# Optimization experiments

Measured on AMD Instinct MI355X. Metric: run time of the kernel, lower is better.

## Reference

```python
import jax, jax.numpy as jnp
import numpy as np

QUERY_DIM = 512
KEY_DIM = 512
NUM_HEADS = 16
HEAD_DIM = QUERY_DIM // NUM_HEADS


def setup_inputs() -> dict:
    key = jax.random.key(0)
    ks = jax.random.split(key, 10)
    B, T, S = 4, 2048, 2048
    s_q = 1.0 / np.sqrt(QUERY_DIM)
    s_k = 1.0 / np.sqrt(KEY_DIM)
    return {
        "x": jax.random.normal(ks[0], (B, T, QUERY_DIM), dtype=jnp.float32),
        "context": jax.random.normal(ks[1], (B, S, KEY_DIM), dtype=jnp.float32),
        "Wq": jax.random.normal(ks[2], (QUERY_DIM, QUERY_DIM), dtype=jnp.float32) * s_q,
        "bq": jnp.zeros((QUERY_DIM,), dtype=jnp.float32),
        "Wk": jax.random.normal(ks[3], (KEY_DIM, QUERY_DIM), dtype=jnp.float32) * s_k,
        "bk": jnp.zeros((QUERY_DIM,), dtype=jnp.float32),
        "Wv": jax.random.normal(ks[4], (KEY_DIM, QUERY_DIM), dtype=jnp.float32) * s_k,
        "bv": jnp.zeros((QUERY_DIM,), dtype=jnp.float32),
        "Wo": jax.random.normal(ks[5], (QUERY_DIM, QUERY_DIM), dtype=jnp.float32) * s_q,
        "bo": jnp.zeros((QUERY_DIM,), dtype=jnp.float32),
    }


def reference(x, context, Wq, bq, Wk, bk, Wv, bv, Wo, bo):
    B, T, C = x.shape
    S = context.shape[1]
    H, D = NUM_HEADS, HEAD_DIM
    scale = D ** -0.5
    # projections -> [B, H, T/S, D]
    q = (x @ Wq + bq).reshape(B, T, H, D).transpose(0, 2, 1, 3)
    k = (context @ Wk + bk).reshape(B, S, H, D).transpose(0, 2, 1, 3)
    v = (context @ Wv + bv).reshape(B, S, H, D).transpose(0, 2, 1, 3)
    # explicit attention matrix [B, H, T, S] (faithful to the unfused original)
    attn = jnp.einsum("bhtd,bhsd->bhts", q, k) * scale
    attn = jax.nn.softmax(attn, axis=-1)  # dropout is identity in eval mode
    out = jnp.einsum("bhts,bhsd->bhtd", attn, v)
    out = out.transpose(0, 2, 1, 3).reshape(B, T, C)
    return out @ Wo + bo
```

## Files before the change

### kernel.cpp

```cpp
#include <hip/hip_runtime.h>
#include <hip/hip_bf16.h>
#include <cmath>

typedef __bf16 bf16;
typedef __bf16 bf16x4 __attribute__((ext_vector_type(4)));
typedef __bf16 bf16x8 __attribute__((ext_vector_type(8)));
typedef float floatx4 __attribute__((ext_vector_type(4)));

#define MFMA_BF16(a, b, c) __builtin_amdgcn_mfma_f32_16x16x32_bf16((a), (b), (c), 0, 0, 0)

#if defined(__has_builtin)
#if __has_builtin(__builtin_amdgcn_global_load_lds)
#define HAVE_GLL 1
#endif
#endif

__device__ __forceinline__ void stage16(const bf16* g, bf16* ldsbase, int lane) {
#ifdef HAVE_GLL
    __builtin_amdgcn_global_load_lds((const __attribute__((address_space(1))) unsigned int*)g,
                                     (__attribute__((address_space(3))) unsigned int*)ldsbase,
                                     16, 0, 0);
#else
    *(int4*)(ldsbase + lane * 8) = *(const int4*)g;
#endif
}

__device__ __forceinline__ int detect_bf16(const void* x) {
    const unsigned short* u = (const unsigned short*)x;
    const int lane = threadIdx.x & 63;
    const unsigned short w0 = u[4 * lane], w1 = u[4 * lane + 2];
    const int e0 = (w0 >> 7) & 0xFF, e1 = (w1 >> 7) & 0xFF;
    const unsigned long long b0 = __ballot(e0 >= 96 && e0 <= 158);
    const unsigned long long b1 = __ballot(e1 >= 96 && e1 <= 158);
    return (__popcll(b0) + __popcll(b1)) >= 90;
}

struct PrepArgs {
    const void* x;
    const void* ctx;
    const void* W[4];
    const void* bias[4];
    bf16* xc;
    bf16* ctxc;
    bf16* WT[4];
    bf16* biasc;
};

__global__ __launch_bounds__(256) void prep(PrepArgs a) {
    const int tid = threadIdx.x;
    const int f = detect_bf16(a.x);
    const int bid = blockIdx.x;
    if (bid < 1024) {
        const int w = bid >> 8, tileid = bid & 255;
        const int bx = tileid & 15, by = tileid >> 4;
        const void* __restrict__ in = a.W[w];
        bf16* __restrict__ out = a.WT[w];
        __shared__ bf16 tile[32][33];
        const int tx = tid & 31, ty = tid >> 5;
        const int x = bx * 32 + tx;
        const int y0 = by * 32;
#pragma unroll
        for (int yy = ty; yy < 32; yy += 8) {
            const size_t idx = (size_t)(y0 + yy) * 512 + x;
            const float v = f ? (float)((const bf16*)in)[idx] : ((const float*)in)[idx];
            tile[yy][tx] = (bf16)v;
        }
        __syncthreads();
        const int xo = by * 32 + tx;
        const int y1 = bx * 32;
#pragma unroll
        for (int yy = ty; yy < 32; yy += 8)
            out[(size_t)(y1 + yy) * 512 + xo] = tile[tx][yy];
    } else if (bid < 5120) {
        const int seg = (bid >= 3072);
        const void* src = seg ? a.ctx : a.x;
        bf16* dst = seg ? a.ctxc : a.xc;
        const int off = (bid - (seg ? 3072 : 1024)) * 256 + tid;
        if (f) {
            ((int4*)dst)[off] = ((const int4*)src)[off];
        } else {
            const float4 p = ((const float4*)src)[2 * off];
            const float4 q = ((const float4*)src)[2 * off + 1];
            bf16x8 o;
            o[0] = (bf16)p.x; o[1] = (bf16)p.y; o[2] = (bf16)p.z; o[3] = (bf16)p.w;
            o[4] = (bf16)q.x; o[5] = (bf16)q.y; o[6] = (bf16)q.z; o[7] = (bf16)q.w;
            *(bf16x8*)(dst + (size_t)off * 8) = o;
        }
    } else {
        for (int e = tid; e < 2048; e += 256) {
            const int seg = e >> 9, off = e & 511;
            const float v =
                f ? (float)((const bf16*)a.bias[seg])[off] : ((const float*)a.bias[seg])[off];
            a.biasc[seg * 512 + off] = (bf16)v;
        }
    }
}

struct QkvArgs {
    const bf16* A[3];
    const bf16* Wt[3];
    const bf16* bias;
    bf16* out[3];
    float scale[3];
};

__global__ __launch_bounds__(256) void gemm_qkv(QkvArgs a) {
    __shared__ __align__(16) bf16 lA[128 * 32];
    __shared__ __align__(16) bf16 lB[128 * 32];
    const int z = blockIdx.z;
    const bf16* __restrict__ A = a.A[z];
    const bf16* __restrict__ Wt = a.Wt[z];
    const int tid = threadIdx.x, wave = tid >> 6, lane = tid & 63;
    const int qd = lane >> 4, j = lane & 15;
    const int m0 = blockIdx.x * 128, n0 = blockIdx.y * 128;
    const int wrow = (wave & 1) * 64, wcol = (wave >> 1) * 64;
    const int srow = wave * 16 + (lane >> 2);
    const int scol = (lane & 3) * 8;
    const bf16* agp = A + (size_t)(m0 + srow) * 512 + scol;
    const bf16* bgp = Wt + (size_t)(n0 + srow) * 512 + scol;
    bf16* lA0 = lA + wave * 512;
    bf16* lB0 = lB + wave * 512;

    floatx4 acc[4][4] = {};

    for (int k0 = 0; k0 < 512; k0 += 32) {
        stage16(agp + k0, lA0, lane);
        stage16(agp + k0 + (size_t)64 * 512, lA0 + 64 * 32, lane);
        stage16(bgp + k0, lB0, lane);
        stage16(bgp + k0 + (size_t)64 * 512, lB0 + 64 * 32, lane);
        __syncthreads();
        bf16x8 af[4], bfr[4];
#pragma unroll
        for (int i = 0; i < 4; ++i) {
            af[i] = *(const bf16x8*)(lA + (wrow + i * 16 + j) * 32 + qd * 8);
            bfr[i] = *(const bf16x8*)(lB + (wcol + i * 16 + j) * 32 + qd * 8);
        }
        if (z < 2) {
#pragma unroll
            for (int nt = 0; nt < 4; ++nt)
#pragma unroll
                for (int rf = 0; rf < 4; ++rf)
                    acc[nt][rf] = MFMA_BF16(bfr[nt], af[rf], acc[nt][rf]);
        } else {
#pragma unroll
            for (int rf = 0; rf < 4; ++rf)
#pragma unroll
                for (int nt = 0; nt < 4; ++nt)
                    acc[rf][nt] = MFMA_BF16(af[rf], bfr[nt], acc[rf][nt]);
        }
        __syncthreads();
    }

    const float scale = a.scale[z];
    const bf16* bias = a.bias + z * 512;
    bf16* __restrict__ C = a.out[z];
    if (z < 2) {
#pragma unroll
        for (int nt = 0; nt < 4; ++nt) {
            const int nb = n0 + wcol + nt * 16 + qd * 4;
            const bf16x4 bv4 = *(const bf16x4*)(bias + nb);
            const int h = nb >> 5, d0 = nb & 31;
#pragma unroll
            for (int rf = 0; rf < 4; ++rf) {
                const int m = m0 + wrow + rf * 16 + j;
                const int bb = m >> 11, t = m & 2047;
                bf16x4 pk;
#pragma unroll
                for (int r = 0; r < 4; ++r)
                    pk[r] = (bf16)((acc[nt][rf][r] + (float)bv4[r]) * scale);
                *(bf16x4*)(&C[(((size_t)bb * 16 + h) * 2048 + t) * 32 + d0]) = pk;
            }
        }
    } else {
#pragma unroll
        for (int nt = 0; nt < 4; ++nt) {
            const int n = n0 + wcol + nt * 16 + j;
            const float bv = (float)bias[n];
            const int h = n >> 5, d = n & 31;
#pragma unroll
            for (int rf = 0; rf < 4; ++rf) {
                const int t0 = m0 + wrow + rf * 16 + qd * 4;
                const int bb = t0 >> 11, s = t0 & 2047;
                bf16x4 pk;
#pragma unroll
                for (int r = 0; r < 4; ++r) pk[r] = (bf16)(acc[rf][nt][r] + bv);
                *(bf16x4*)(&C[(((size_t)bb * 16 + h) * 32 + d) * 2048 + s]) = pk;
            }
        }
    }
}

__global__ __launch_bounds__(256) void gemm_out(const bf16* __restrict__ A,
                                                const bf16* __restrict__ Wt,
                                                const bf16* __restrict__ bias,
                                                void* __restrict__ C,
                                                const void* __restrict__ xorig) {
    __shared__ __align__(16) bf16 lA[128 * 32];
    __shared__ __align__(16) bf16 lB[128 * 32];
    const int oflag = detect_bf16(xorig);
    const int tid = threadIdx.x, wave = tid >> 6, lane = tid & 63;
    const int qd = lane >> 4, j = lane & 15;
    const int m0 = blockIdx.x * 128, n0 = blockIdx.y * 128;
    const int wrow = (wave & 1) * 64, wcol = (wave >> 1) * 64;
    const int srow = wave * 16 + (lane >> 2);
    const int scol = (lane & 3) * 8;
    const bf16* agp = A + (size_t)(m0 + srow) * 512 + scol;
    const bf16* bgp = Wt + (size_t)(n0 + srow) * 512 + scol;
    bf16* lA0 = lA + wave * 512;
    bf16* lB0 = lB + wave * 512;

    floatx4 acc[4][4] = {};

    for (int k0 = 0; k0 < 512; k0 += 32) {
        stage16(agp + k0, lA0, lane);
        stage16(agp + k0 + (size_t)64 * 512, lA0 + 64 * 32, lane);
        stage16(bgp + k0, lB0, lane);
        stage16(bgp + k0 + (size_t)64 * 512, lB0 + 64 * 32, lane);
        __syncthreads();
        bf16x8 af[4], bfr[4];
#pragma unroll
        for (int i = 0; i < 4; ++i) {
            af[i] = *(const bf16x8*)(lA + (wrow + i * 16 + j) * 32 + qd * 8);
            bfr[i] = *(const bf16x8*)(lB + (wcol + i * 16 + j) * 32 + qd * 8);
        }
#pragma unroll
        for (int nt = 0; nt < 4; ++nt)
#pragma unroll
            for (int rf = 0; rf < 4; ++rf)
                acc[nt][rf] = MFMA_BF16(bfr[nt], af[rf], acc[nt][rf]);
        __syncthreads();
    }

#pragma unroll
    for (int nt = 0; nt < 4; ++nt) {
        const int nb = n0 + wcol + nt * 16 + qd * 4;
        const bf16x4 bv4 = *(const bf16x4*)(bias + nb);
#pragma unroll
        for (int rf = 0; rf < 4; ++rf) {
            const int m = m0 + wrow + rf * 16 + j;
            if (oflag) {
                bf16x4 pk;
#pragma unroll
                for (int r = 0; r < 4; ++r) pk[r] = (bf16)(acc[nt][rf][r] + (float)bv4[r]);
                *(bf16x4*)((bf16*)C + (size_t)m * 512 + nb) = pk;
            } else {
                float4 v;
                v.x = acc[nt][rf][0] + (float)bv4[0];
                v.y = acc[nt][rf][1] + (float)bv4[1];
                v.z = acc[nt][rf][2] + (float)bv4[2];
                v.w = acc[nt][rf][3] + (float)bv4[3];
                *(float4*)((float*)C + (size_t)m * 512 + nb) = v;
            }
        }
    }
}

__global__ __launch_bounds__(256) void attn_kernel(const bf16* __restrict__ Q,
                                                   const bf16* __restrict__ Kh,
                                                   const bf16* __restrict__ Vt,
                                                   bf16* __restrict__ O) {
    const int tid = threadIdx.x;
    const int wave = tid >> 6, lane = tid & 63;
    const int qd = lane >> 4, j = lane & 15;
    const int bh = blockIdx.y;
    const int b = bh >> 4, h = bh & 15;
    const int tw = blockIdx.x * 256 + wave * 64;

    __shared__ __align__(16) bf16 lP[4][64 * 68];
    bf16* lp = lP[wave];

    const bf16* qbase = Q + ((size_t)bh * 2048 + tw) * 32;
    const bf16* kbase = Kh + (size_t)bh * 2048 * 32;
    const bf16* vbase = Vt + (size_t)bh * 32 * 2048;

    bf16x8 qf[4];
#pragma unroll
    for (int tf = 0; tf < 4; ++tf)
        qf[tf] = *(const bf16x8*)(qbase + (size_t)(tf * 16 + j) * 32 + qd * 8);

    const floatx4 zero = {0.f, 0.f, 0.f, 0.f};
    floatx4 oacc[4][2] = {};
    float lrow[4] = {0.f, 0.f, 0.f, 0.f};

    bf16x8 kc[4], vc[4], kn[4], vn[4], vp[4];

    auto loadK = [&](int s0, bf16x8* k) {
#pragma unroll
        for (int sf = 0; sf < 4; ++sf)
            k[sf] = *(const bf16x8*)(kbase + (size_t)(s0 + sf * 16 + j) * 32 + qd * 8);
    };
    auto loadV = [&](int s0, bf16x8* v) {
#pragma unroll
        for (int dt = 0; dt < 2; ++dt)
#pragma unroll
            for (int kk = 0; kk < 2; ++kk)
                v[dt * 2 + kk] =
                    *(const bf16x8*)(vbase + (size_t)(dt * 16 + j) * 2048 + s0 + kk * 32 + qd * 8);
    };
    auto qk_exp_write = [&](bf16x8* k) {
#pragma unroll
        for (int sf = 0; sf < 4; ++sf)
#pragma unroll
            for (int tf = 0; tf < 4; ++tf) {
                const floatx4 sc = MFMA_BF16(k[sf], qf[tf], zero);
                float e0 = __builtin_amdgcn_exp2f(sc[0]);
                float e1 = __builtin_amdgcn_exp2f(sc[1]);
                float e2 = __builtin_amdgcn_exp2f(sc[2]);
                float e3 = __builtin_amdgcn_exp2f(sc[3]);
                lrow[tf] += (e0 + e1) + (e2 + e3);
                bf16x4 pk;
                pk[0] = (bf16)e0; pk[1] = (bf16)e1; pk[2] = (bf16)e2; pk[3] = (bf16)e3;
                *(bf16x4*)(lp + (tf * 16 + j) * 68 + sf * 16 + qd * 4) = pk;
            }
    };
    auto pv = [&](bf16x8* v) {
#pragma unroll
        for (int rf = 0; rf < 4; ++rf)
#pragma unroll
            for (int kk = 0; kk < 2; ++kk) {
                const bf16x8 pf = *(const bf16x8*)(lp + (rf * 16 + j) * 68 + kk * 32 + qd * 8);
#pragma unroll
                for (int dt = 0; dt < 2; ++dt)
                    oacc[rf][dt] = MFMA_BF16(pf, v[dt * 2 + kk], oacc[rf][dt]);
            }
    };

    loadK(0, kc);
    loadV(0, vc);
    qk_exp_write(kc);
#pragma unroll
    for (int i = 0; i < 4; ++i) vp[i] = vc[i];
    loadK(64, kc);
    loadV(64, vc);

    for (int it = 1; it < 32; ++it) {
        const int sn = (it + 1) * 64 & 2047;
        loadK(sn, kn);
        loadV(sn, vn);
        pv(vp);
        qk_exp_write(kc);
#pragma unroll
        for (int i = 0; i < 4; ++i) { vp[i] = vc[i]; kc[i] = kn[i]; vc[i] = vn[i]; }
    }
    pv(vp);

    float lr[4];
#pragma unroll
    for (int tf = 0; tf < 4; ++tf) {
        float v = lrow[tf];
        v += __shfl_xor(v, 16);
        v += __shfl_xor(v, 32);
        lr[tf] = v;
    }

#pragma unroll
    for (int rf = 0; rf < 4; ++rf)
#pragma unroll
        for (int r = 0; r < 4; ++r) {
            const float den = __shfl(lr[rf], qd * 4 + r);
            const float inv = 1.0f / den;
            const int t = tw + rf * 16 + qd * 4 + r;
#pragma unroll
            for (int dt = 0; dt < 2; ++dt)
                O[((size_t)b * 2048 + t) * 512 + h * 32 + dt * 16 + j] =
                    (bf16)(oacc[rf][dt][r] * inv);
        }
}

extern "C" void kernel_launch(void* const* d_in, const int* in_sizes, int n_in, void* d_out,
                              int out_size, void* d_ws, size_t ws_size, hipStream_t stream) {
    char* ws = (char*)d_ws;
    bf16* wqT = (bf16*)(ws + 1048576);
    bf16* wkT = (bf16*)(ws + 1572864);
    bf16* wvT = (bf16*)(ws + 2097152);
    bf16* woT = (bf16*)(ws + 2621440);
    bf16* biasc = (bf16*)(ws + 3145728);
    bf16* xc = (bf16*)(ws + 4194304);
    bf16* ctxc = (bf16*)(ws + 12582912);
    bf16* qws = (bf16*)(ws + 20971520);
    bf16* kws = (bf16*)(ws + 29360128);
    bf16* vtws = (bf16*)(ws + 37748736);
    bf16* aws = xc;

    PrepArgs pa;
    pa.x = d_in[0]; pa.ctx = d_in[1];
    pa.W[0] = d_in[2]; pa.W[1] = d_in[4]; pa.W[2] = d_in[6]; pa.W[3] = d_in[8];
    pa.bias[0] = d_in[3]; pa.bias[1] = d_in[5]; pa.bias[2] = d_in[7]; pa.bias[3] = d_in[9];
    pa.xc = xc; pa.ctxc = ctxc;
    pa.WT[0] = wqT; pa.WT[1] = wkT; pa.WT[2] = wvT; pa.WT[3] = woT;
    pa.biasc = biasc;
    prep<<<5121, 256, 0, stream>>>(pa);

    QkvArgs qa;
    qa.A[0] = xc; qa.A[1] = ctxc; qa.A[2] = ctxc;
    qa.Wt[0] = wqT; qa.Wt[1] = wkT; qa.Wt[2] = wvT;
    qa.bias = biasc;
    qa.out[0] = qws; qa.out[1] = kws; qa.out[2] = vtws;
    qa.scale[0] = 0.2550348593f; qa.scale[1] = 1.0f; qa.scale[2] = 1.0f;
    gemm_qkv<<<dim3(64, 4, 3), 256, 0, stream>>>(qa);

    attn_kernel<<<dim3(8, 64), 256, 0, stream>>>(qws, kws, vtws, aws);

    gemm_out<<<dim3(64, 4), 256, 0, stream>>>(aws, woT, biasc + 3 * 512, d_out, d_in[0]);
}
```

Before: 218.0 us.

## Split attention over the key dimension and merge partials inside the output GEMM

```diff
diff --git a/kernel.cpp b/kernel.cpp
--- a/kernel.cpp
+++ b/kernel.cpp
@@ -72,20 +72,17 @@
         for (int yy = ty; yy < 32; yy += 8)
             out[(size_t)(y1 + yy) * 512 + xo] = tile[tx][yy];
     } else if (bid < 5120) {
+        if (f) return;
         const int seg = (bid >= 3072);
         const void* src = seg ? a.ctx : a.x;
         bf16* dst = seg ? a.ctxc : a.xc;
         const int off = (bid - (seg ? 3072 : 1024)) * 256 + tid;
-        if (f) {
-            ((int4*)dst)[off] = ((const int4*)src)[off];
-        } else {
-            const float4 p = ((const float4*)src)[2 * off];
-            const float4 q = ((const float4*)src)[2 * off + 1];
-            bf16x8 o;
-            o[0] = (bf16)p.x; o[1] = (bf16)p.y; o[2] = (bf16)p.z; o[3] = (bf16)p.w;
-            o[4] = (bf16)q.x; o[5] = (bf16)q.y; o[6] = (bf16)q.z; o[7] = (bf16)q.w;
-            *(bf16x8*)(dst + (size_t)off * 8) = o;
-        }
+        const float4 p = ((const float4*)src)[2 * off];
+        const float4 q = ((const float4*)src)[2 * off + 1];
+        bf16x8 o;
+        o[0] = (bf16)p.x; o[1] = (bf16)p.y; o[2] = (bf16)p.z; o[3] = (bf16)p.w;
+        o[4] = (bf16)q.x; o[5] = (bf16)q.y; o[6] = (bf16)q.z; o[7] = (bf16)q.w;
+        *(bf16x8*)(dst + (size_t)off * 8) = o;
     } else {
         for (int e = tid; e < 2048; e += 256) {
             const int seg = e >> 9, off = e & 511;
@@ -97,7 +94,9 @@
 }
 
 struct QkvArgs {
-    const bf16* A[3];
+    const void* xraw;
+    const void* ctxraw;
+    const bf16* Aconv[3];
     const bf16* Wt[3];
     const bf16* bias;
     bf16* out[3];
@@ -108,7 +107,9 @@
     __shared__ __align__(16) bf16 lA[128 * 32];
     __shared__ __align__(16) bf16 lB[128 * 32];
     const int z = blockIdx.z;
-    const bf16* __restrict__ A = a.A[z];
+    const int f = detect_bf16(a.xraw);
+    const bf16* __restrict__ A =
+        f ? (const bf16*)(z == 0 ? a.xraw : a.ctxraw) : a.Aconv[z];
     const bf16* __restrict__ Wt = a.Wt[z];
     const int tid = threadIdx.x, wave = tid >> 6, lane = tid & 63;
     const int qd = lane >> 4, j = lane & 15;
@@ -190,81 +191,20 @@
     }
 }
 
-__global__ __launch_bounds__(256) void gemm_out(const bf16* __restrict__ A,
-                                                const bf16* __restrict__ Wt,
-                                                const bf16* __restrict__ bias,
-                                                void* __restrict__ C,
-                                                const void* __restrict__ xorig) {
-    __shared__ __align__(16) bf16 lA[128 * 32];
-    __shared__ __align__(16) bf16 lB[128 * 32];
-    const int oflag = detect_bf16(xorig);
-    const int tid = threadIdx.x, wave = tid >> 6, lane = tid & 63;
-    const int qd = lane >> 4, j = lane & 15;
-    const int m0 = blockIdx.x * 128, n0 = blockIdx.y * 128;
-    const int wrow = (wave & 1) * 64, wcol = (wave >> 1) * 64;
-    const int srow = wave * 16 + (lane >> 2);
-    const int scol = (lane & 3) * 8;
-    const bf16* agp = A + (size_t)(m0 + srow) * 512 + scol;
-    const bf16* bgp = Wt + (size_t)(n0 + srow) * 512 + scol;
-    bf16* lA0 = lA + wave * 512;
-    bf16* lB0 = lB + wave * 512;
-
-    floatx4 acc[4][4] = {};
-
-    for (int k0 = 0; k0 < 512; k0 += 32) {
-        stage16(agp + k0, lA0, lane);
-        stage16(agp + k0 + (size_t)64 * 512, lA0 + 64 * 32, lane);
-        stage16(bgp + k0, lB0, lane);
-        stage16(bgp + k0 + (size_t)64 * 512, lB0 + 64 * 32, lane);
-        __syncthreads();
-        bf16x8 af[4], bfr[4];
-#pragma unroll
-        for (int i = 0; i < 4; ++i) {
-            af[i] = *(const bf16x8*)(lA + (wrow + i * 16 + j) * 32 + qd * 8);
-            bfr[i] = *(const bf16x8*)(lB + (wcol + i * 16 + j) * 32 + qd * 8);
-        }
-#pragma unroll
-        for (int nt = 0; nt < 4; ++nt)
-#pragma unroll
-            for (int rf = 0; rf < 4; ++rf)
-                acc[nt][rf] = MFMA_BF16(bfr[nt], af[rf], acc[nt][rf]);
-        __syncthreads();
-    }
-
-#pragma unroll
-    for (int nt = 0; nt < 4; ++nt) {
-        const int nb = n0 + wcol + nt * 16 + qd * 4;
-        const bf16x4 bv4 = *(const bf16x4*)(bias + nb);
-#pragma unroll
-        for (int rf = 0; rf < 4; ++rf) {
-            const int m = m0 + wrow + rf * 16 + j;
-            if (oflag) {
-                bf16x4 pk;
-#pragma unroll
-                for (int r = 0; r < 4; ++r) pk[r] = (bf16)(acc[nt][rf][r] + (float)bv4[r]);
-                *(bf16x4*)((bf16*)C + (size_t)m * 512 + nb) = pk;
-            } else {
-                float4 v;
-                v.x = acc[nt][rf][0] + (float)bv4[0];
-                v.y = acc[nt][rf][1] + (float)bv4[1];
-                v.z = acc[nt][rf][2] + (float)bv4[2];
-                v.w = acc[nt][rf][3] + (float)bv4[3];
-                *(float4*)((float*)C + (size_t)m * 512 + nb) = v;
-            }
-        }
-    }
-}
-
 __global__ __launch_bounds__(256) void attn_kernel(const bf16* __restrict__ Q,
                                                    const bf16* __restrict__ Kh,
                                                    const bf16* __restrict__ Vt,
-                                                   bf16* __restrict__ O) {
+                                                   bf16* __restrict__ Opart,
+                                                   float* __restrict__ lpart)
+{
     const int tid = threadIdx.x;
     const int wave = tid >> 6, lane = tid & 63;
     const int qd = lane >> 4, j = lane & 15;
-    const int bh = blockIdx.y;
+    const int bh = blockIdx.x;
     const int b = bh >> 4, h = bh & 15;
-    const int tw = blockIdx.x * 256 + wave * 64;
+    const int tw = blockIdx.y * 256 + wave * 64;
+    const int z = blockIdx.z;
+    const int sbase = z * 1024;
 
     __shared__ __align__(16) bf16 lP[4][64 * 68];
     bf16* lp = lP[wave];
@@ -325,16 +265,16 @@
             }
     };
 
-    loadK(0, kc);
-    loadV(0, vc);
+    loadK(sbase, kc);
+    loadV(sbase, vc);
     qk_exp_write(kc);
 #pragma unroll
     for (int i = 0; i < 4; ++i) vp[i] = vc[i];
-    loadK(64, kc);
-    loadV(64, vc);
-
-    for (int it = 1; it < 32; ++it) {
-        const int sn = (it + 1) * 64 & 2047;
+    loadK(sbase + 64, kc);
+    loadV(sbase + 64, vc);
+
+    for (int it = 1; it < 16; ++it) {
+        const int sn = sbase + (((it + 1) * 64) & 1023);
         loadK(sn, kn);
         loadV(sn, vn);
         pv(vp);
@@ -353,23 +293,108 @@
         lr[tf] = v;
     }
 
+    bf16* op = Opart + (size_t)z * 8192 * 512;
+    float* lo = lpart + (size_t)z * 131072 + (size_t)bh * 2048 + tw;
+    if (qd == 0) {
+#pragma unroll
+        for (int tf = 0; tf < 4; ++tf) lo[tf * 16 + j] = lr[tf];
+    }
 #pragma unroll
     for (int rf = 0; rf < 4; ++rf)
 #pragma unroll
         for (int r = 0; r < 4; ++r) {
-            const float den = __shfl(lr[rf], qd * 4 + r);
-            const float inv = 1.0f / den;
             const int t = tw + rf * 16 + qd * 4 + r;
 #pragma unroll
             for (int dt = 0; dt < 2; ++dt)
-                O[((size_t)b * 2048 + t) * 512 + h * 32 + dt * 16 + j] =
-                    (bf16)(oacc[rf][dt][r] * inv);
-        }
+                op[((size_t)b * 2048 + t) * 512 + h * 32 + dt * 16 + j] =
+                    (bf16)oacc[rf][dt][r];
+        }
+}
+
+__global__ __launch_bounds__(256) void inv_l_kernel(float* __restrict__ l) {
+    const int i = blockIdx.x * 256 + threadIdx.x;
+    l[i] = 1.0f / (l[i] + l[i + 131072]);
+}
+
+__global__ __launch_bounds__(256) void gemm_out(const bf16* __restrict__ O01,
+                                                const float* __restrict__ invl,
+                                                const bf16* __restrict__ Wt,
+                                                const bf16* __restrict__ bias,
+                                                void* __restrict__ C,
+                                                const void* __restrict__ xraw) {
+    __shared__ __align__(16) bf16 lA[64 * 32];
+    __shared__ __align__(16) bf16 lB[128 * 32];
+    const int oflag = detect_bf16(xraw);
+    const int tid = threadIdx.x, wave = tid >> 6, lane = tid & 63;
+    const int qd = lane >> 4, j = lane & 15;
+    const int m0 = blockIdx.x * 64, n0 = blockIdx.y * 128;
+    const int srow = tid >> 2;
+    const int scol = (tid & 3) * 8;
+    const int m = m0 + srow;
+    const int bb = m >> 11, t = m & 2047;
+    const bf16* o0p = O01 + (size_t)m * 512 + scol;
+    const bf16* o1p = o0p + (size_t)8192 * 512;
+    const float* invp = invl + (size_t)bb * 16 * 2048 + t;
+    const int srowB = wave * 16 + (lane >> 2);
+    const bf16* bgp = Wt + (size_t)(n0 + srowB) * 512 + scol;
+    bf16* lB0 = lB + wave * 512;
+
+    floatx4 acc[2][4] = {};
+
+    for (int k0 = 0; k0 < 512; k0 += 32) {
+        stage16(bgp + k0, lB0, lane);
+        stage16(bgp + k0 + (size_t)64 * 512, lB0 + 64 * 32, lane);
+        const bf16x8 o0 = *(const bf16x8*)(o0p + k0);
+        const bf16x8 o1 = *(const bf16x8*)(o1p + k0);
+        const float iv = invp[(k0 >> 5) * 2048];
+        bf16x8 av;
+#pragma unroll
+        for (int e = 0; e < 8; ++e) av[e] = (bf16)(((float)o0[e] + (float)o1[e]) * iv);
+        *(bf16x8*)(lA + srow * 32 + scol) = av;
+        __syncthreads();
+        bf16x8 af[4], bf2[2];
+#pragma unroll
+        for (int rf = 0; rf < 4; ++rf)
+            af[rf] = *(const bf16x8*)(lA + (rf * 16 + j) * 32 + qd * 8);
+#pragma unroll
+        for (int nt = 0; nt < 2; ++nt)
+            bf2[nt] = *(const bf16x8*)(lB + (wave * 32 + nt * 16 + j) * 32 + qd * 8);
+#pragma unroll
+        for (int nt = 0; nt < 2; ++nt)
+#pragma unroll
+            for (int rf = 0; rf < 4; ++rf)
+                acc[nt][rf] = MFMA_BF16(bf2[nt], af[rf], acc[nt][rf]);
+        __syncthreads();
+    }
+
+#pragma unroll
+    for (int nt = 0; nt < 2; ++nt) {
+        const int nb = n0 + wave * 32 + nt * 16 + qd * 4;
+        const bf16x4 bv4 = *(const bf16x4*)(bias + nb);
+#pragma unroll
+        for (int rf = 0; rf < 4; ++rf) {
+            const int mm = m0 + rf * 16 + j;
+            if (oflag) {
+                bf16x4 pk;
+#pragma unroll
+                for (int r = 0; r < 4; ++r) pk[r] = (bf16)(acc[nt][rf][r] + (float)bv4[r]);
+                *(bf16x4*)((bf16*)C + (size_t)mm * 512 + nb) = pk;
+            } else {
+                float4 v;
+                v.x = acc[nt][rf][0] + (float)bv4[0];
+                v.y = acc[nt][rf][1] + (float)bv4[1];
+                v.z = acc[nt][rf][2] + (float)bv4[2];
+                v.w = acc[nt][rf][3] + (float)bv4[3];
+                *(float4*)((float*)C + (size_t)mm * 512 + nb) = v;
+            }
+        }
+    }
 }
 
 extern "C" void kernel_launch(void* const* d_in, const int* in_sizes, int n_in, void* d_out,
                               int out_size, void* d_ws, size_t ws_size, hipStream_t stream) {
     char* ws = (char*)d_ws;
+    float* lpart = (float*)(ws + 0);
     bf16* wqT = (bf16*)(ws + 1048576);
     bf16* wkT = (bf16*)(ws + 1572864);
     bf16* wvT = (bf16*)(ws + 2097152);
@@ -380,7 +405,7 @@
     bf16* qws = (bf16*)(ws + 20971520);
     bf16* kws = (bf16*)(ws + 29360128);
     bf16* vtws = (bf16*)(ws + 37748736);
-    bf16* aws = xc;
+    bf16* Oparts = xc;
 
     PrepArgs pa;
     pa.x = d_in[0]; pa.ctx = d_in[1];
@@ -392,14 +417,18 @@
     prep<<<5121, 256, 0, stream>>>(pa);
 
     QkvArgs qa;
-    qa.A[0] = xc; qa.A[1] = ctxc; qa.A[2] = ctxc;
+    qa.xraw = d_in[0]; qa.ctxraw = d_in[1];
+    qa.Aconv[0] = xc; qa.Aconv[1] = ctxc; qa.Aconv[2] = ctxc;
     qa.Wt[0] = wqT; qa.Wt[1] = wkT; qa.Wt[2] = wvT;
     qa.bias = biasc;
     qa.out[0] = qws; qa.out[1] = kws; qa.out[2] = vtws;
     qa.scale[0] = 0.2550348593f; qa.scale[1] = 1.0f; qa.scale[2] = 1.0f;
     gemm_qkv<<<dim3(64, 4, 3), 256, 0, stream>>>(qa);
 
-    attn_kernel<<<dim3(8, 64), 256, 0, stream>>>(qws, kws, vtws, aws);
-
-    gemm_out<<<dim3(64, 4), 256, 0, stream>>>(aws, woT, biasc + 3 * 512, d_out, d_in[0]);
-}
+    attn_kernel<<<dim3(64, 8, 2), 256, 0, stream>>>(qws, kws, vtws, Oparts, lpart);
+
+    inv_l_kernel<<<512, 256, 0, stream>>>(lpart);
+
+    gemm_out<<<dim3(128, 4), 256, 0, stream>>>(Oparts, lpart, woT, biasc + 3 * 512, d_out,
+                                               d_in[0]);
+}
```

Result: slower. 226.7 us (+4.0%).

## Shrink attention tiles to 32 query rows per wave and double-buffer K/V explicitly

Applied to the files above, without the earlier changes.

```diff
diff --git a/kernel.cpp b/kernel.cpp
--- a/kernel.cpp
+++ b/kernel.cpp
@@ -72,20 +72,17 @@
         for (int yy = ty; yy < 32; yy += 8)
             out[(size_t)(y1 + yy) * 512 + xo] = tile[tx][yy];
     } else if (bid < 5120) {
+        if (f) return;
         const int seg = (bid >= 3072);
         const void* src = seg ? a.ctx : a.x;
         bf16* dst = seg ? a.ctxc : a.xc;
         const int off = (bid - (seg ? 3072 : 1024)) * 256 + tid;
-        if (f) {
-            ((int4*)dst)[off] = ((const int4*)src)[off];
-        } else {
-            const float4 p = ((const float4*)src)[2 * off];
-            const float4 q = ((const float4*)src)[2 * off + 1];
-            bf16x8 o;
-            o[0] = (bf16)p.x; o[1] = (bf16)p.y; o[2] = (bf16)p.z; o[3] = (bf16)p.w;
-            o[4] = (bf16)q.x; o[5] = (bf16)q.y; o[6] = (bf16)q.z; o[7] = (bf16)q.w;
-            *(bf16x8*)(dst + (size_t)off * 8) = o;
-        }
+        const float4 p = ((const float4*)src)[2 * off];
+        const float4 q = ((const float4*)src)[2 * off + 1];
+        bf16x8 o;
+        o[0] = (bf16)p.x; o[1] = (bf16)p.y; o[2] = (bf16)p.z; o[3] = (bf16)p.w;
+        o[4] = (bf16)q.x; o[5] = (bf16)q.y; o[6] = (bf16)q.z; o[7] = (bf16)q.w;
+        *(bf16x8*)(dst + (size_t)off * 8) = o;
     } else {
         for (int e = tid; e < 2048; e += 256) {
             const int seg = e >> 9, off = e & 511;
@@ -97,7 +94,9 @@
 }
 
 struct QkvArgs {
-    const bf16* A[3];
+    const void* xraw;
+    const void* ctxraw;
+    const bf16* Aconv[3];
     const bf16* Wt[3];
     const bf16* bias;
     bf16* out[3];
@@ -108,7 +107,9 @@
     __shared__ __align__(16) bf16 lA[128 * 32];
     __shared__ __align__(16) bf16 lB[128 * 32];
     const int z = blockIdx.z;
-    const bf16* __restrict__ A = a.A[z];
+    const int f = detect_bf16(a.xraw);
+    const bf16* __restrict__ A =
+        f ? (const bf16*)(z == 0 ? a.xraw : a.ctxraw) : a.Aconv[z];
     const bf16* __restrict__ Wt = a.Wt[z];
     const int tid = threadIdx.x, wave = tid >> 6, lane = tid & 63;
     const int qd = lane >> 4, j = lane & 15;
@@ -190,71 +191,6 @@
     }
 }
 
-__global__ __launch_bounds__(256) void gemm_out(const bf16* __restrict__ A,
-                                                const bf16* __restrict__ Wt,
-                                                const bf16* __restrict__ bias,
-                                                void* __restrict__ C,
-                                                const void* __restrict__ xorig) {
-    __shared__ __align__(16) bf16 lA[128 * 32];
-    __shared__ __align__(16) bf16 lB[128 * 32];
-    const int oflag = detect_bf16(xorig);
-    const int tid = threadIdx.x, wave = tid >> 6, lane = tid & 63;
-    const int qd = lane >> 4, j = lane & 15;
-    const int m0 = blockIdx.x * 128, n0 = blockIdx.y * 128;
-    const int wrow = (wave & 1) * 64, wcol = (wave >> 1) * 64;
-    const int srow = wave * 16 + (lane >> 2);
-    const int scol = (lane & 3) * 8;
-    const bf16* agp = A + (size_t)(m0 + srow) * 512 + scol;
-    const bf16* bgp = Wt + (size_t)(n0 + srow) * 512 + scol;
-    bf16* lA0 = lA + wave * 512;
-    bf16* lB0 = lB + wave * 512;
-
-    floatx4 acc[4][4] = {};
-
-    for (int k0 = 0; k0 < 512; k0 += 32) {
-        stage16(agp + k0, lA0, lane);
-        stage16(agp + k0 + (size_t)64 * 512, lA0 + 64 * 32, lane);
-        stage16(bgp + k0, lB0, lane);
-        stage16(bgp + k0 + (size_t)64 * 512, lB0 + 64 * 32, lane);
-        __syncthreads();
-        bf16x8 af[4], bfr[4];
-#pragma unroll
-        for (int i = 0; i < 4; ++i) {
-            af[i] = *(const bf16x8*)(lA + (wrow + i * 16 + j) * 32 + qd * 8);
-            bfr[i] = *(const bf16x8*)(lB + (wcol + i * 16 + j) * 32 + qd * 8);
-        }
-#pragma unroll
-        for (int nt = 0; nt < 4; ++nt)
-#pragma unroll
-            for (int rf = 0; rf < 4; ++rf)
-                acc[nt][rf] = MFMA_BF16(bfr[nt], af[rf], acc[nt][rf]);
-        __syncthreads();
-    }
-
-#pragma unroll
-    for (int nt = 0; nt < 4; ++nt) {
-        const int nb = n0 + wcol + nt * 16 + qd * 4;
-        const bf16x4 bv4 = *(const bf16x4*)(bias + nb);
-#pragma unroll
-        for (int rf = 0; rf < 4; ++rf) {
-            const int m = m0 + wrow + rf * 16 + j;
-            if (oflag) {
-                bf16x4 pk;
-#pragma unroll
-                for (int r = 0; r < 4; ++r) pk[r] = (bf16)(acc[nt][rf][r] + (float)bv4[r]);
-                *(bf16x4*)((bf16*)C + (size_t)m * 512 + nb) = pk;
-            } else {
-                float4 v;
-                v.x = acc[nt][rf][0] + (float)bv4[0];
-                v.y = acc[nt][rf][1] + (float)bv4[1];
-                v.z = acc[nt][rf][2] + (float)bv4[2];
-                v.w = acc[nt][rf][3] + (float)bv4[3];
-                *(float4*)((float*)C + (size_t)m * 512 + nb) = v;
-            }
-        }
-    }
-}
-
 __global__ __launch_bounds__(256) void attn_kernel(const bf16* __restrict__ Q,
                                                    const bf16* __restrict__ Kh,
                                                    const bf16* __restrict__ Vt,
@@ -262,27 +198,27 @@
     const int tid = threadIdx.x;
     const int wave = tid >> 6, lane = tid & 63;
     const int qd = lane >> 4, j = lane & 15;
-    const int bh = blockIdx.y;
+    const int bh = blockIdx.x;
     const int b = bh >> 4, h = bh & 15;
-    const int tw = blockIdx.x * 256 + wave * 64;
-
-    __shared__ __align__(16) bf16 lP[4][64 * 68];
+    const int tw = blockIdx.y * 128 + wave * 32;
+
+    __shared__ __align__(16) bf16 lP[4][32 * 68];
     bf16* lp = lP[wave];
 
     const bf16* qbase = Q + ((size_t)bh * 2048 + tw) * 32;
     const bf16* kbase = Kh + (size_t)bh * 2048 * 32;
     const bf16* vbase = Vt + (size_t)bh * 32 * 2048;
 
-    bf16x8 qf[4];
-#pragma unroll
-    for (int tf = 0; tf < 4; ++tf)
+    bf16x8 qf[2];
+#pragma unroll
+    for (int tf = 0; tf < 2; ++tf)
         qf[tf] = *(const bf16x8*)(qbase + (size_t)(tf * 16 + j) * 32 + qd * 8);
 
     const floatx4 zero = {0.f, 0.f, 0.f, 0.f};
-    floatx4 oacc[4][2] = {};
-    float lrow[4] = {0.f, 0.f, 0.f, 0.f};
-
-    bf16x8 kc[4], vc[4], kn[4], vn[4], vp[4];
+    floatx4 oacc[2][2] = {};
+    float lrow[2] = {0.f, 0.f};
+
+    bf16x8 K0[4], K1[4], V0[4], V1[4];
 
     auto loadK = [&](int s0, bf16x8* k) {
 #pragma unroll
@@ -297,11 +233,11 @@
                 v[dt * 2 + kk] =
                     *(const bf16x8*)(vbase + (size_t)(dt * 16 + j) * 2048 + s0 + kk * 32 + qd * 8);
     };
-    auto qk_exp_write = [&](bf16x8* k) {
+    auto qk = [&](bf16x8* k) {
 #pragma unroll
         for (int sf = 0; sf < 4; ++sf)
 #pragma unroll
-            for (int tf = 0; tf < 4; ++tf) {
+            for (int tf = 0; tf < 2; ++tf) {
                 const floatx4 sc = MFMA_BF16(k[sf], qf[tf], zero);
                 float e0 = __builtin_amdgcn_exp2f(sc[0]);
                 float e1 = __builtin_amdgcn_exp2f(sc[1]);
@@ -315,7 +251,7 @@
     };
     auto pv = [&](bf16x8* v) {
 #pragma unroll
-        for (int rf = 0; rf < 4; ++rf)
+        for (int rf = 0; rf < 2; ++rf)
 #pragma unroll
             for (int kk = 0; kk < 2; ++kk) {
                 const bf16x8 pf = *(const bf16x8*)(lp + (rf * 16 + j) * 68 + kk * 32 + qd * 8);
@@ -325,28 +261,29 @@
             }
     };
 
-    loadK(0, kc);
-    loadV(0, vc);
-    qk_exp_write(kc);
-#pragma unroll
-    for (int i = 0; i < 4; ++i) vp[i] = vc[i];
-    loadK(64, kc);
-    loadV(64, vc);
-
-    for (int it = 1; it < 32; ++it) {
-        const int sn = (it + 1) * 64 & 2047;
-        loadK(sn, kn);
-        loadV(sn, vn);
-        pv(vp);
-        qk_exp_write(kc);
-#pragma unroll
-        for (int i = 0; i < 4; ++i) { vp[i] = vc[i]; kc[i] = kn[i]; vc[i] = vn[i]; }
-    }
-    pv(vp);
-
-    float lr[4];
-#pragma unroll
-    for (int tf = 0; tf < 4; ++tf) {
+    loadK(0, K0);
+    loadV(0, V0);
+    qk(K0);
+    loadK(64, K1);
+    for (int k = 1; k <= 15; ++k) {
+        const int c = 2 * k - 1;
+        loadV(c * 64, V1);
+        pv(V0);
+        qk(K1);
+        loadK((c + 1) * 64, K0);
+        loadV((c + 1) * 64, V0);
+        pv(V1);
+        qk(K0);
+        loadK((c + 2) * 64, K1);
+    }
+    loadV(31 * 64, V1);
+    pv(V0);
+    qk(K1);
+    pv(V1);
+
+    float lr[2];
+#pragma unroll
+    for (int tf = 0; tf < 2; ++tf) {
         float v = lrow[tf];
         v += __shfl_xor(v, 16);
         v += __shfl_xor(v, 32);
@@ -354,7 +291,7 @@
     }
 
 #pragma unroll
-    for (int rf = 0; rf < 4; ++rf)
+    for (int rf = 0; rf < 2; ++rf)
 #pragma unroll
         for (int r = 0; r < 4; ++r) {
             const float den = __shfl(lr[rf], qd * 4 + r);
@@ -365,6 +302,71 @@
                 O[((size_t)b * 2048 + t) * 512 + h * 32 + dt * 16 + j] =
                     (bf16)(oacc[rf][dt][r] * inv);
         }
+}
+
+__global__ __launch_bounds__(256) void gemm_out(const bf16* __restrict__ A,
+                                                const bf16* __restrict__ Wt,
+                                                const bf16* __restrict__ bias,
+                                                void* __restrict__ C,
+                                                const void* __restrict__ xraw) {
+    __shared__ __align__(16) bf16 lA[128 * 32];
+    __shared__ __align__(16) bf16 lB[128 * 32];
+    const int oflag = detect_bf16(xraw);
+    const int tid = threadIdx.x, wave = tid >> 6, lane = tid & 63;
+    const int qd = lane >> 4, j = lane & 15;
+    const int m0 = blockIdx.x * 128, n0 = blockIdx.y * 128;
+    const int wrow = (wave & 1) * 64, wcol = (wave >> 1) * 64;
+    const int srow = wave * 16 + (lane >> 2);
+    const int scol = (lane & 3) * 8;
+    const bf16* agp = A + (size_t)(m0 + srow) * 512 + scol;
+    const bf16* bgp = Wt + (size_t)(n0 + srow) * 512 + scol;
+    bf16* lA0 = lA + wave * 512;
+    bf16* lB0 = lB + wave * 512;
+
+    floatx4 acc[4][4] = {};
+
+    for (int k0 = 0; k0 < 512; k0 += 32) {
+        stage16(agp + k0, lA0, lane);
+        stage16(agp + k0 + (size_t)64 * 512, lA0 + 64 * 32, lane);
+        stage16(bgp + k0, lB0, lane);
+        stage16(bgp + k0 + (size_t)64 * 512, lB0 + 64 * 32, lane);
+        __syncthreads();
+        bf16x8 af[4], bfr[4];
+#pragma unroll
+        for (int i = 0; i < 4; ++i) {
+            af[i] = *(const bf16x8*)(lA + (wrow + i * 16 + j) * 32 + qd * 8);
+            bfr[i] = *(const bf16x8*)(lB + (wcol + i * 16 + j) * 32 + qd * 8);
+        }
+#pragma unroll
+        for (int nt = 0; nt < 4; ++nt)
+#pragma unroll
+            for (int rf = 0; rf < 4; ++rf)
+                acc[nt][rf] = MFMA_BF16(bfr[nt], af[rf], acc[nt][rf]);
+        __syncthreads();
+    }
+
+#pragma unroll
+    for (int nt = 0; nt < 4; ++nt) {
+        const int nb = n0 + wcol + nt * 16 + qd * 4;
+        const bf16x4 bv4 = *(const bf16x4*)(bias + nb);
+#pragma unroll
+        for (int rf = 0; rf < 4; ++rf) {
+            const int m = m0 + wrow + rf * 16 + j;
+            if (oflag) {
+                bf16x4 pk;
+#pragma unroll
+                for (int r = 0; r < 4; ++r) pk[r] = (bf16)(acc[nt][rf][r] + (float)bv4[r]);
+                *(bf16x4*)((bf16*)C + (size_t)m * 512 + nb) = pk;
+            } else {
+                float4 v;
+                v.x = acc[nt][rf][0] + (float)bv4[0];
+                v.y = acc[nt][rf][1] + (float)bv4[1];
+                v.z = acc[nt][rf][2] + (float)bv4[2];
+                v.w = acc[nt][rf][3] + (float)bv4[3];
+                *(float4*)((float*)C + (size_t)m * 512 + nb) = v;
+            }
+        }
+    }
 }
 
 extern "C" void kernel_launch(void* const* d_in, const int* in_sizes, int n_in, void* d_out,
@@ -392,14 +394,15 @@
     prep<<<5121, 256, 0, stream>>>(pa);
 
     QkvArgs qa;
-    qa.A[0] = xc; qa.A[1] = ctxc; qa.A[2] = ctxc;
+    qa.xraw = d_in[0]; qa.ctxraw = d_in[1];
+    qa.Aconv[0] = xc; qa.Aconv[1] = ctxc; qa.Aconv[2] = ctxc;
     qa.Wt[0] = wqT; qa.Wt[1] = wkT; qa.Wt[2] = wvT;
     qa.bias = biasc;
     qa.out[0] = qws; qa.out[1] = kws; qa.out[2] = vtws;
     qa.scale[0] = 0.2550348593f; qa.scale[1] = 1.0f; qa.scale[2] = 1.0f;
     gemm_qkv<<<dim3(64, 4, 3), 256, 0, stream>>>(qa);
 
-    attn_kernel<<<dim3(8, 64), 256, 0, stream>>>(qws, kws, vtws, aws);
+    attn_kernel<<<dim3(64, 16), 256, 0, stream>>>(qws, kws, vtws, aws);
 
     gemm_out<<<dim3(64, 4), 256, 0, stream>>>(aws, woT, biasc + 3 * 512, d_out, d_in[0]);
 }
```

After: 232.5 us. +6.7%, slower.
